# Optimization experiments

Hardware: AMD Instinct MI355X
Metric: run time of the kernel (lower is better)

## Reference

```python
import jax, jax.numpy as jnp
import numpy as np

N, C, H, K = 100000, 64, 8, 16
D = C // H  # head_dim = 8


def setup_inputs() -> dict:
    key = jax.random.key(0)
    ks = jax.random.split(key, 7)
    s = 1.0 / np.sqrt(C)
    return {
        "feats": jax.random.normal(ks[0], (N, C), jnp.float32),
        "knn_idx": jax.random.randint(ks[1], (N, K), 0, N, jnp.int32),
        "Wq": jax.random.normal(ks[2], (C, C), jnp.float32) * s,
        "Wk": jax.random.normal(ks[3], (C, C), jnp.float32) * s,
        "Wv": jax.random.normal(ks[4], (C, C), jnp.float32) * s,
        "Wo": jax.random.normal(ks[5], (C, C), jnp.float32) * s,
        "bo": jnp.zeros((C,), jnp.float32),
    }


def reference(feats, knn_idx, Wq, Wk, Wv, Wo, bo):
    # Projections (torch Linear y = x @ W^T expressed with pre-transposed W)
    q = (feats @ Wq).reshape(N, H, D)          # [N,H,D]
    k_feat = (feats @ Wk).reshape(N, H, D)     # [N,H,D]
    v = (feats @ Wv).reshape(N, H, D)          # [N,H,D]

    # Gather k-NN neighbors: [N,K,H,D]
    k_nb = k_feat[knn_idx]
    v_nb = v[knn_idx]

    # Scores: dot(q, k_neighbor) per head, scaled
    scores = jnp.einsum("nhd,nkhd->nkh", q, k_nb) / np.sqrt(D).astype(np.float32)
    attn = jax.nn.softmax(scores, axis=1)      # softmax over K neighbors

    out = jnp.einsum("nkh,nkhd->nhd", attn, v_nb).reshape(N, C)
    return out @ Wo + bo
```

## Files before the change

### kernel.cpp

```cpp
#include <hip/hip_runtime.h>
#include <hip/hip_fp16.h>
#include <math.h>

#define NPTS 100000
#define CDIM 64
#define KNN  16

typedef unsigned int uint;
typedef _Float16 f16x8 __attribute__((ext_vector_type(8)));
typedef float    f32x4 __attribute__((ext_vector_type(4)));

template <int CTRL>
__device__ __forceinline__ float dpp_add(float x) {
    int yi = __builtin_amdgcn_mov_dpp(__float_as_int(x), CTRL, 0xF, 0xF, true);
    return x + __int_as_float(yi);
}


__global__ __launch_bounds__(256) void pack_w(
    const float* __restrict__ Wq, const float* __restrict__ Wk,
    const float* __restrict__ Wv, const float* __restrict__ Wo,
    __half* __restrict__ frag)
{
    const float* Ws[4] = {Wq, Wk, Wv, Wo};
    f16x8* fp = (f16x8*)frag;
    for (int e = threadIdx.x; e < 2048; e += 256) {
        const int lane = e & 63;
        const int ks   = (e >> 6) & 1;
        const int ct   = (e >> 7) & 3;
        const int mat  = e >> 9;
        const int m = lane & 15, quad = lane >> 4;
        const float* W = Ws[mat];
        f16x8 b;
        #pragma unroll
        for (int j = 0; j < 8; ++j)
            b[j] = (_Float16)W[(size_t)(ks * 32 + quad * 8 + j) * 64 + ct * 16 + m];
        fp[e] = b;
    }
}

__device__ __forceinline__ f16x8 load_afrag(const float* fp, int ks, int quad) {
    const float4 x0 = *(const float4*)(fp + ks * 32 + quad * 8);
    const float4 x1 = *(const float4*)(fp + ks * 32 + quad * 8 + 4);
    f16x8 a;
    a[0] = (_Float16)x0.x; a[1] = (_Float16)x0.y;
    a[2] = (_Float16)x0.z; a[3] = (_Float16)x0.w;
    a[4] = (_Float16)x1.x; a[5] = (_Float16)x1.y;
    a[6] = (_Float16)x1.z; a[7] = (_Float16)x1.w;
    return a;
}

__global__ __launch_bounds__(256) void proj_qkv(
    const float* __restrict__ feats, const __half* __restrict__ frag,
    __half* __restrict__ q, uint* __restrict__ kv)
{
    const int wid = blockIdx.x * 4 + (threadIdx.x >> 6);
    if (wid >= NPTS / 16) return;
    const int lane = threadIdx.x & 63;
    const int m = lane & 15, quad = lane >> 4;

    const f16x8* fp = (const f16x8*)frag;
    f16x8 Bf[3][4][2];
    #pragma unroll
    for (int mat = 0; mat < 3; ++mat)
        #pragma unroll
        for (int ct = 0; ct < 4; ++ct)
            #pragma unroll
            for (int ks = 0; ks < 2; ++ks)
                Bf[mat][ct][ks] = fp[((mat * 4 + ct) * 2 + ks) * 64 + lane];

    const int r0 = wid * 16;
    const float* ap = feats + (size_t)(r0 + m) * 64;
    const f16x8 Af0 = load_afrag(ap, 0, quad);
    const f16x8 Af1 = load_afrag(ap, 1, quad);

    #pragma unroll
    for (int ct = 0; ct < 4; ++ct) {
        f32x4 aq = {0.f, 0.f, 0.f, 0.f};
        f32x4 ak = {0.f, 0.f, 0.f, 0.f};
        f32x4 av = {0.f, 0.f, 0.f, 0.f};
        aq = __builtin_amdgcn_mfma_f32_16x16x32_f16(Af0, Bf[0][ct][0], aq, 0, 0, 0);
        aq = __builtin_amdgcn_mfma_f32_16x16x32_f16(Af1, Bf[0][ct][1], aq, 0, 0, 0);
        ak = __builtin_amdgcn_mfma_f32_16x16x32_f16(Af0, Bf[1][ct][0], ak, 0, 0, 0);
        ak = __builtin_amdgcn_mfma_f32_16x16x32_f16(Af1, Bf[1][ct][1], ak, 0, 0, 0);
        av = __builtin_amdgcn_mfma_f32_16x16x32_f16(Af0, Bf[2][ct][0], av, 0, 0, 0);
        av = __builtin_amdgcn_mfma_f32_16x16x32_f16(Af1, Bf[2][ct][1], av, 0, 0, 0);

        const int col = ct * 16 + m;
        #pragma unroll
        for (int r = 0; r < 4; ++r) {
            const size_t off = (size_t)(r0 + quad * 4 + r) * 64 + col;
            q[off] = __float2half(aq[r]);
            kv[off] = (uint)__half_as_ushort(__float2half(ak[r]))
                    | ((uint)__half_as_ushort(__float2half(av[r])) << 16);
        }
    }
}

__global__ __launch_bounds__(256) void attn_out(
    const __half* __restrict__ q, const uint* __restrict__ kv,
    const int* __restrict__ knn, const __half* __restrict__ frag,
    const float* __restrict__ bo, float* __restrict__ out)
{
    __shared__ float sO[16][68];
    const int t = threadIdx.x;
    const int lane = t & 63;
    const int w = t >> 6;
    const int m = lane & 15, quad = lane >> 4;

    const f16x8* fpb = (const f16x8*)frag;
    const f16x8 Wf0 = fpb[((3 * 4 + w) * 2 + 0) * 64 + lane];
    const f16x8 Wf1 = fpb[((3 * 4 + w) * 2 + 1) * 64 + lane];
    const float bias = bo[w * 16 + m];

    const int n0 = blockIdx.x * 16;

    #pragma unroll 1
    for (int p = 0; p < 4; ++p) {
        const int n = n0 + w * 4 + p;
        const int ns = __builtin_amdgcn_readfirstlane(n);

        const float qv = __half2float(q[(size_t)n * 64 + lane]);

        const int* kr = knn + (size_t)ns * KNN;
        int idx[KNN];
        #pragma unroll
        for (int i = 0; i < KNN; ++i) idx[i] = kr[i];

        float sc[KNN], vr[KNN];
        #pragma unroll
        for (int i = 0; i < KNN; ++i) {
            const uint wv = kv[(size_t)idx[i] * 64 + lane];
            const float2 kvf = __half22float2(*(const __half2*)&wv);
            vr[i] = kvf.y;
            float pr = qv * kvf.x;
            pr = dpp_add<0xB1>(pr);
            pr = dpp_add<0x4E>(pr);
            pr = dpp_add<0x141>(pr);
            sc[i] = pr * 0.3535533905932738f;
        }

        float mx = sc[0];
        #pragma unroll
        for (int i = 1; i < KNN; ++i) mx = fmaxf(mx, sc[i]);
        float s = 0.f;
        #pragma unroll
        for (int i = 0; i < KNN; ++i) { sc[i] = __expf(sc[i] - mx); s += sc[i]; }
        const float inv = 1.f / s;

        float acc = 0.f;
        #pragma unroll
        for (int i = 0; i < KNN; ++i) acc += sc[i] * vr[i];

        sO[w * 4 + p][lane] = acc * inv;
    }
    __syncthreads();

    const float* ap = &sO[m][0];
    f16x8 Af0, Af1;
    {
        const float4 x0 = *(const float4*)(ap + quad * 8);
        const float4 x1 = *(const float4*)(ap + quad * 8 + 4);
        Af0[0] = (_Float16)x0.x; Af0[1] = (_Float16)x0.y;
        Af0[2] = (_Float16)x0.z; Af0[3] = (_Float16)x0.w;
        Af0[4] = (_Float16)x1.x; Af0[5] = (_Float16)x1.y;
        Af0[6] = (_Float16)x1.z; Af0[7] = (_Float16)x1.w;
        const float4 y0 = *(const float4*)(ap + 32 + quad * 8);
        const float4 y1 = *(const float4*)(ap + 32 + quad * 8 + 4);
        Af1[0] = (_Float16)y0.x; Af1[1] = (_Float16)y0.y;
        Af1[2] = (_Float16)y0.z; Af1[3] = (_Float16)y0.w;
        Af1[4] = (_Float16)y1.x; Af1[5] = (_Float16)y1.y;
        Af1[6] = (_Float16)y1.z; Af1[7] = (_Float16)y1.w;
    }

    f32x4 ac = {0.f, 0.f, 0.f, 0.f};
    ac = __builtin_amdgcn_mfma_f32_16x16x32_f16(Af0, Wf0, ac, 0, 0, 0);
    ac = __builtin_amdgcn_mfma_f32_16x16x32_f16(Af1, Wf1, ac, 0, 0, 0);

    const int col = w * 16 + m;
    #pragma unroll
    for (int r = 0; r < 4; ++r)
        out[(size_t)(n0 + quad * 4 + r) * 64 + col] = ac[r] + bias;
}

extern "C" void kernel_launch(void* const* d_in, const int* in_sizes, int n_in,
                              void* d_out, int out_size, void* d_ws, size_t ws_size,
                              hipStream_t stream) {
    const float* feats = (const float*)d_in[0];
    const int*   knn   = (const int*)d_in[1];
    const float* Wq    = (const float*)d_in[2];
    const float* Wk    = (const float*)d_in[3];
    const float* Wv    = (const float*)d_in[4];
    const float* Wo    = (const float*)d_in[5];
    const float* bo    = (const float*)d_in[6];
    float* out = (float*)d_out;

    __half* frag = (__half*)d_ws;
    __half* q_h  = (__half*)((char*)d_ws + 32768);
    uint*   kvb  = (uint*)((char*)d_ws + 32768 +
                           (size_t)NPTS * CDIM * sizeof(__half));

    pack_w<<<1, 256, 0, stream>>>(Wq, Wk, Wv, Wo, frag);
    proj_qkv<<<(NPTS / 16 + 3) / 4, 256, 0, stream>>>(feats, frag, q_h, kvb);
    attn_out<<<NPTS / 16, 256, 0, stream>>>(q_h, kvb, knn, frag, bo, out);
}
```

Before: 158.2 us.

## Swap MFMA operands for vectorized stores, drop softmax max, parallelize weight packing

The MFMA operand order is swapped (weights as A, features as B), so each lane holds four consecutive output channels of a single point. The q, kv and output stores can then be packed into uint2/uint4/float4 vector writes instead of scattered scalar writes. Softmax drops the max-subtraction pass and computes exp2 directly on scores prescaled by log2(e), which risks overflow for large scores. Weight packing now runs on 8 blocks instead of looping within one block.

Result: slower. 194.4 us (+22.9%).

```diff
diff --git a/kernel.cpp b/kernel.cpp
--- a/kernel.cpp
+++ b/kernel.cpp
@@ -24,22 +24,21 @@
 {
     const float* Ws[4] = {Wq, Wk, Wv, Wo};
     f16x8* fp = (f16x8*)frag;
-    for (int e = threadIdx.x; e < 2048; e += 256) {
-        const int lane = e & 63;
-        const int ks   = (e >> 6) & 1;
-        const int ct   = (e >> 7) & 3;
-        const int mat  = e >> 9;
-        const int m = lane & 15, quad = lane >> 4;
-        const float* W = Ws[mat];
-        f16x8 b;
-        #pragma unroll
-        for (int j = 0; j < 8; ++j)
-            b[j] = (_Float16)W[(size_t)(ks * 32 + quad * 8 + j) * 64 + ct * 16 + m];
-        fp[e] = b;
-    }
-}
-
-__device__ __forceinline__ f16x8 load_afrag(const float* fp, int ks, int quad) {
+    const int e = blockIdx.x * 256 + threadIdx.x;
+    const int lane = e & 63;
+    const int ks   = (e >> 6) & 1;
+    const int ct   = (e >> 7) & 3;
+    const int mat  = e >> 9;
+    const int m = lane & 15, quad = lane >> 4;
+    const float* W = Ws[mat];
+    f16x8 b;
+    #pragma unroll
+    for (int j = 0; j < 8; ++j)
+        b[j] = (_Float16)W[(size_t)(ks * 32 + quad * 8 + j) * 64 + ct * 16 + m];
+    fp[e] = b;
+}
+
+__device__ __forceinline__ f16x8 load_bfeat(const float* fp, int ks, int quad) {
     const float4 x0 = *(const float4*)(fp + ks * 32 + quad * 8);
     const float4 x1 = *(const float4*)(fp + ks * 32 + quad * 8 + 4);
     f16x8 a;
@@ -60,40 +59,51 @@
     const int m = lane & 15, quad = lane >> 4;
 
     const f16x8* fp = (const f16x8*)frag;
-    f16x8 Bf[3][4][2];
+    f16x8 Wf[3][4][2];
     #pragma unroll
     for (int mat = 0; mat < 3; ++mat)
         #pragma unroll
         for (int ct = 0; ct < 4; ++ct)
             #pragma unroll
             for (int ks = 0; ks < 2; ++ks)
-                Bf[mat][ct][ks] = fp[((mat * 4 + ct) * 2 + ks) * 64 + lane];
+                Wf[mat][ct][ks] = fp[((mat * 4 + ct) * 2 + ks) * 64 + lane];
 
     const int r0 = wid * 16;
     const float* ap = feats + (size_t)(r0 + m) * 64;
-    const f16x8 Af0 = load_afrag(ap, 0, quad);
-    const f16x8 Af1 = load_afrag(ap, 1, quad);
+    const f16x8 Bf0 = load_bfeat(ap, 0, quad);
+    const f16x8 Bf1 = load_bfeat(ap, 1, quad);
+
+    const size_t pt = (size_t)(r0 + m);
 
     #pragma unroll
     for (int ct = 0; ct < 4; ++ct) {
         f32x4 aq = {0.f, 0.f, 0.f, 0.f};
         f32x4 ak = {0.f, 0.f, 0.f, 0.f};
         f32x4 av = {0.f, 0.f, 0.f, 0.f};
-        aq = __builtin_amdgcn_mfma_f32_16x16x32_f16(Af0, Bf[0][ct][0], aq, 0, 0, 0);
-        aq = __builtin_amdgcn_mfma_f32_16x16x32_f16(Af1, Bf[0][ct][1], aq, 0, 0, 0);
-        ak = __builtin_amdgcn_mfma_f32_16x16x32_f16(Af0, Bf[1][ct][0], ak, 0, 0, 0);
-        ak = __builtin_amdgcn_mfma_f32_16x16x32_f16(Af1, Bf[1][ct][1], ak, 0, 0, 0);
-        av = __builtin_amdgcn_mfma_f32_16x16x32_f16(Af0, Bf[2][ct][0], av, 0, 0, 0);
-        av = __builtin_amdgcn_mfma_f32_16x16x32_f16(Af1, Bf[2][ct][1], av, 0, 0, 0);
-
-        const int col = ct * 16 + m;
-        #pragma unroll
-        for (int r = 0; r < 4; ++r) {
-            const size_t off = (size_t)(r0 + quad * 4 + r) * 64 + col;
-            q[off] = __float2half(aq[r]);
-            kv[off] = (uint)__half_as_ushort(__float2half(ak[r]))
-                    | ((uint)__half_as_ushort(__float2half(av[r])) << 16);
-        }
+        aq = __builtin_amdgcn_mfma_f32_16x16x32_f16(Wf[0][ct][0], Bf0, aq, 0, 0, 0);
+        aq = __builtin_amdgcn_mfma_f32_16x16x32_f16(Wf[0][ct][1], Bf1, aq, 0, 0, 0);
+        ak = __builtin_amdgcn_mfma_f32_16x16x32_f16(Wf[1][ct][0], Bf0, ak, 0, 0, 0);
+        ak = __builtin_amdgcn_mfma_f32_16x16x32_f16(Wf[1][ct][1], Bf1, ak, 0, 0, 0);
+        av = __builtin_amdgcn_mfma_f32_16x16x32_f16(Wf[2][ct][0], Bf0, av, 0, 0, 0);
+        av = __builtin_amdgcn_mfma_f32_16x16x32_f16(Wf[2][ct][1], Bf1, av, 0, 0, 0);
+
+        const int ch = ct * 16 + quad * 4;
+        uint2 qp;
+        qp.x = (uint)__half_as_ushort(__float2half(aq[0]))
+             | ((uint)__half_as_ushort(__float2half(aq[1])) << 16);
+        qp.y = (uint)__half_as_ushort(__float2half(aq[2]))
+             | ((uint)__half_as_ushort(__float2half(aq[3])) << 16);
+        *(uint2*)(q + pt * 64 + ch) = qp;
+        uint4 kp;
+        kp.x = (uint)__half_as_ushort(__float2half(ak[0]))
+             | ((uint)__half_as_ushort(__float2half(av[0])) << 16);
+        kp.y = (uint)__half_as_ushort(__float2half(ak[1]))
+             | ((uint)__half_as_ushort(__float2half(av[1])) << 16);
+        kp.z = (uint)__half_as_ushort(__float2half(ak[2]))
+             | ((uint)__half_as_ushort(__float2half(av[2])) << 16);
+        kp.w = (uint)__half_as_ushort(__float2half(ak[3]))
+             | ((uint)__half_as_ushort(__float2half(av[3])) << 16);
+        *(uint4*)(kv + pt * 64 + ch) = kp;
     }
 }
 
@@ -111,9 +121,9 @@
     const f16x8* fpb = (const f16x8*)frag;
     const f16x8 Wf0 = fpb[((3 * 4 + w) * 2 + 0) * 64 + lane];
     const f16x8 Wf1 = fpb[((3 * 4 + w) * 2 + 1) * 64 + lane];
-    const float bias = bo[w * 16 + m];
 
     const int n0 = blockIdx.x * 16;
+    const float SC = 0.3535533905932738f * 1.4426950408889634f;
 
     #pragma unroll 1
     for (int p = 0; p < 4; ++p) {
@@ -137,15 +147,12 @@
             pr = dpp_add<0xB1>(pr);
             pr = dpp_add<0x4E>(pr);
             pr = dpp_add<0x141>(pr);
-            sc[i] = pr * 0.3535533905932738f;
+            sc[i] = __builtin_amdgcn_exp2f(pr * SC);
         }
 
-        float mx = sc[0];
-        #pragma unroll
-        for (int i = 1; i < KNN; ++i) mx = fmaxf(mx, sc[i]);
         float s = 0.f;
         #pragma unroll
-        for (int i = 0; i < KNN; ++i) { sc[i] = __expf(sc[i] - mx); s += sc[i]; }
+        for (int i = 0; i < KNN; ++i) s += sc[i];
         const float inv = 1.f / s;
 
         float acc = 0.f;
@@ -156,31 +163,33 @@
     }
     __syncthreads();
 
-    const float* ap = &sO[m][0];
-    f16x8 Af0, Af1;
+    f16x8 Bf0, Bf1;
     {
+        const float* ap = &sO[m][0];
         const float4 x0 = *(const float4*)(ap + quad * 8);
         const float4 x1 = *(const float4*)(ap + quad * 8 + 4);
-        Af0[0] = (_Float16)x0.x; Af0[1] = (_Float16)x0.y;
-        Af0[2] = (_Float16)x0.z; Af0[3] = (_Float16)x0.w;
-        Af0[4] = (_Float16)x1.x; Af0[5] = (_Float16)x1.y;
-        Af0[6] = (_Float16)x1.z; Af0[7] = (_Float16)x1.w;
+        Bf0[0] = (_Float16)x0.x; Bf0[1] = (_Float16)x0.y;
+        Bf0[2] = (_Float16)x0.z; Bf0[3] = (_Float16)x0.w;
+        Bf0[4] = (_Float16)x1.x; Bf0[5] = (_Float16)x1.y;
+        Bf0[6] = (_Float16)x1.z; Bf0[7] = (_Float16)x1.w;
         const float4 y0 = *(const float4*)(ap + 32 + quad * 8);
         const float4 y1 = *(const float4*)(ap + 32 + quad * 8 + 4);
-        Af1[0] = (_Float16)y0.x; Af1[1] = (_Float16)y0.y;
-        Af1[2] = (_Float16)y0.z; Af1[3] = (_Float16)y0.w;
-        Af1[4] = (_Float16)y1.x; Af1[5] = (_Float16)y1.y;
-        Af1[6] = (_Float16)y1.z; Af1[7] = (_Float16)y1.w;
+        Bf1[0] = (_Float16)y0.x; Bf1[1] = (_Float16)y0.y;
+        Bf1[2] = (_Float16)y0.z; Bf1[3] = (_Float16)y0.w;
+        Bf1[4] = (_Float16)y1.x; Bf1[5] = (_Float16)y1.y;
+        Bf1[6] = (_Float16)y1.z; Bf1[7] = (_Float16)y1.w;
     }
 
     f32x4 ac = {0.f, 0.f, 0.f, 0.f};
-    ac = __builtin_amdgcn_mfma_f32_16x16x32_f16(Af0, Wf0, ac, 0, 0, 0);
-    ac = __builtin_amdgcn_mfma_f32_16x16x32_f16(Af1, Wf1, ac, 0, 0, 0);
-
-    const int col = w * 16 + m;
-    #pragma unroll
-    for (int r = 0; r < 4; ++r)
-        out[(size_t)(n0 + quad * 4 + r) * 64 + col] = ac[r] + bias;
+    ac = __builtin_amdgcn_mfma_f32_16x16x32_f16(Wf0, Bf0, ac, 0, 0, 0);
+    ac = __builtin_amdgcn_mfma_f32_16x16x32_f16(Wf1, Bf1, ac, 0, 0, 0);
+
+    const int ch = w * 16 + quad * 4;
+    const float4 bias = *(const float4*)(bo + ch);
+    float4 o;
+    o.x = ac[0] + bias.x; o.y = ac[1] + bias.y;
+    o.z = ac[2] + bias.z; o.w = ac[3] + bias.w;
+    *(float4*)(out + (size_t)(n0 + m) * 64 + ch) = o;
 }
 
 extern "C" void kernel_launch(void* const* d_in, const int* in_sizes, int n_in,
@@ -200,7 +209,7 @@
     uint*   kvb  = (uint*)((char*)d_ws + 32768 +
                            (size_t)NPTS * CDIM * sizeof(__half));
 
-    pack_w<<<1, 256, 0, stream>>>(Wq, Wk, Wv, Wo, frag);
+    pack_w<<<8, 256, 0, stream>>>(Wq, Wk, Wv, Wo, frag);
     proj_qkv<<<(NPTS / 16 + 3) / 4, 256, 0, stream>>>(feats, frag, q_h, kvb);
     attn_out<<<NPTS / 16, 256, 0, stream>>>(q_h, kvb, knn, frag, bo, out);
 }
```
